# Kernel optimization log

Measured on AMD Instinct MI355X. Metric: run time of the kernel, lower is better.

## Reference

```python
import jax, jax.numpy as jnp
import numpy as np

B, T, N, D_IN = 2, 64, 64, 512
HID, L, H = 256, 2, 4
C = HID // H  # 64 per-head channels
NEG_SLOPE = 0.2
LN_EPS = 1e-5


def setup_inputs() -> dict:
    key = jax.random.key(0)
    ks = jax.random.split(key, 8)
    s_in = 1.0 / np.sqrt(D_IN)
    s_h = 1.0 / np.sqrt(HID)
    s_c = 1.0 / np.sqrt(C)
    return {
        "x": jax.random.normal(ks[0], (B, T, N, D_IN), jnp.float32),
        "person_mask": jax.random.randint(ks[1], (B, T, N), 0, 2) > 0,
        "W_in": (jax.random.normal(ks[2], (D_IN, HID)) * s_in).astype(jnp.float32),
        "b_in": jnp.zeros((HID,), jnp.float32),
        "Wl": (jax.random.normal(ks[3], (L, HID, HID)) * s_h).astype(jnp.float32),
        "bl": jnp.zeros((L, HID), jnp.float32),
        "Wr": (jax.random.normal(ks[4], (L, HID, HID)) * s_h).astype(jnp.float32),
        "br": jnp.zeros((L, HID), jnp.float32),
        "att": (jax.random.normal(ks[5], (L, H, C)) * s_c).astype(jnp.float32),
        "out_bias": jnp.zeros((L, HID), jnp.float32),
        "ln_scale": jnp.ones((L, HID), jnp.float32),
        "ln_bias": jnp.zeros((L, HID), jnp.float32),
    }


def _layernorm(x, g, b):
    mu = jnp.mean(x, axis=-1, keepdims=True)
    var = jnp.mean(jnp.square(x - mu), axis=-1, keepdims=True)
    return (x - mu) * jax.lax.rsqrt(var + LN_EPS) * g + b


def _gatv2_layer(h, allowed, Wl, bl, Wr, br, att, ob):
    # h: [bt, N, HID]; allowed: [bt, N, N] bool (edge j->i at [b,i,j])
    bt, n, _ = h.shape
    xl = (h @ Wl + bl).reshape(bt, n, H, C)  # source features (messages)
    xr = (h @ Wr + br).reshape(bt, n, H, C)  # target features
    # GATv2 logit: e_ij = a . leaky_relu(xr_i + xl_j), per head
    s = xr[:, :, None, :, :] + xl[:, None, :, :, :]  # [bt, i, j, H, C]
    e = jnp.einsum('bijhc,hc->bijh', jax.nn.leaky_relu(s, NEG_SLOPE), att)
    e = jnp.where(allowed[..., None], e, -1e9)
    alpha = jax.nn.softmax(e, axis=2)  # segment softmax over incoming edges j
    out = jnp.einsum('bijh,bjhc->bihc', alpha, xl)  # weighted scatter-sum
    return out.reshape(bt, n, H * C) + ob


def _forward(x, person_mask, W_in, b_in, Wl, bl, Wr, br, att, out_bias, ln_scale, ln_bias):
    b, t, n, _ = x.shape
    bt = b * t
    h = (x @ W_in + b_in).reshape(bt, n, HID)
    m = person_mask.reshape(bt, n)
    # edges: all pairs among masked nodes (incl. diag) + self loops for every node
    allowed = (m[:, :, None] & m[:, None, :]) | jnp.eye(n, dtype=bool)[None]
    hi = h
    for li in range(L):
        res = hi
        g = _gatv2_layer(hi, allowed, Wl[li], bl[li], Wr[li], br[li], att[li], out_bias[li])
        g = jax.nn.elu(g)  # dropout is identity in eval mode
        g = _layernorm(g, ln_scale[li], ln_bias[li])
        hi = g + res  # use_residual=True
        hi = jnp.where(m[:, :, None], hi, 0.0)
    # graphs with <=1 masked node are skipped (pass through projected features)
    keep = (jnp.sum(m, axis=-1) > 1)[:, None, None]
    out = jnp.where(keep, hi, h)
    return out.reshape(b, t, n, HID)


def reference(x, person_mask, W_in, b_in, Wl, bl, Wr, br, att, out_bias, ln_scale, ln_bias):
    return _forward(x, person_mask, W_in, b_in, Wl, bl, Wr, br, att, out_bias, ln_scale, ln_bias)
```

## Files before the change

### kernel.cpp

```cpp
#include <hip/hip_runtime.h>
#include <hip/hip_bf16.h>

#define BT_G   128
#define NND    64
#define D_IN_  512
#define HID_   256
#define NH     4
#define NCH    64
#define NROWS  8192
#define LN_EPS_    1e-5f

typedef __hip_bfloat16 bf16;
typedef __attribute__((ext_vector_type(8))) short short8;
typedef __attribute__((ext_vector_type(4))) float float4v;

union PrepArena {
    float t[32][33];
    struct { bf16 As[64 * 72]; bf16 Bs[64 * 72]; } g;
    int flags[4];
};

__global__ __launch_bounds__(256) void prep_gemm_in_kernel(
    const float* __restrict__ x, const unsigned* __restrict__ mw,
    const float* __restrict__ W_in, const float* __restrict__ b_in,
    const float* __restrict__ Wl, const float* __restrict__ Wr,
    float* __restrict__ Cf, bf16* __restrict__ Cb16,
    bf16* __restrict__ WlrT, int* __restrict__ mout)
{
    __shared__ PrepArena ar;
    const int tid = threadIdx.x;
    const int bid = blockIdx.x;

    if (bid < 512) {
        bf16* As = ar.g.As;
        bf16* Bs = ar.g.Bs;
        const int wave = tid >> 6, lane = tid & 63;
        const int quad = lane >> 4, l16 = lane & 15;
        const int m0 = (bid >> 2) * 64, n0 = (bid & 3) * 64;
        const int wm = (wave & 1) * 32, wn = (wave >> 1) * 32;
        float4v acc[2][2] = {};
        const int r  = tid >> 2;
        const int cq = (tid & 3) * 16;
        for (int k0 = 0; k0 < D_IN_; k0 += 64) {
            const float* sa = x + (size_t)(m0 + r) * D_IN_ + k0 + cq;
            const float4 f0 = *(const float4*)(sa);
            const float4 f1 = *(const float4*)(sa + 4);
            const float4 f2 = *(const float4*)(sa + 8);
            const float4 f3 = *(const float4*)(sa + 12);
            const float* sw = W_in + (size_t)(k0 + r) * HID_ + n0 + cq;
            float wv[16];
            *(float4*)(wv)      = *(const float4*)(sw);
            *(float4*)(wv + 4)  = *(const float4*)(sw + 4);
            *(float4*)(wv + 8)  = *(const float4*)(sw + 8);
            *(float4*)(wv + 12) = *(const float4*)(sw + 12);
            union { bf16 hh[16]; float4 v[2]; } u;
            u.hh[0]=__float2bfloat16(f0.x); u.hh[1]=__float2bfloat16(f0.y);
            u.hh[2]=__float2bfloat16(f0.z); u.hh[3]=__float2bfloat16(f0.w);
            u.hh[4]=__float2bfloat16(f1.x); u.hh[5]=__float2bfloat16(f1.y);
            u.hh[6]=__float2bfloat16(f1.z); u.hh[7]=__float2bfloat16(f1.w);
            u.hh[8]=__float2bfloat16(f2.x); u.hh[9]=__float2bfloat16(f2.y);
            u.hh[10]=__float2bfloat16(f2.z); u.hh[11]=__float2bfloat16(f2.w);
            u.hh[12]=__float2bfloat16(f3.x); u.hh[13]=__float2bfloat16(f3.y);
            u.hh[14]=__float2bfloat16(f3.z); u.hh[15]=__float2bfloat16(f3.w);
            __syncthreads();
            *(float4*)(&As[r * 72 + cq])     = u.v[0];
            *(float4*)(&As[r * 72 + cq + 8]) = u.v[1];
            #pragma unroll
            for (int j = 0; j < 16; ++j)
                Bs[(cq + j) * 72 + r] = __float2bfloat16(wv[j]);
            __syncthreads();
            #pragma unroll
            for (int kk = 0; kk < 64; kk += 32) {
                short8 af[2], bf2[2];
                #pragma unroll
                for (int mi = 0; mi < 2; ++mi)
                    af[mi] = *(const short8*)(&As[(wm + mi * 16 + l16) * 72 + kk + quad * 8]);
                #pragma unroll
                for (int ni = 0; ni < 2; ++ni)
                    bf2[ni] = *(const short8*)(&Bs[(wn + ni * 16 + l16) * 72 + kk + quad * 8]);
                #pragma unroll
                for (int mi = 0; mi < 2; ++mi)
                    #pragma unroll
                    for (int ni = 0; ni < 2; ++ni)
                        acc[mi][ni] = __builtin_amdgcn_mfma_f32_16x16x32_bf16(
                            af[mi], bf2[ni], acc[mi][ni], 0, 0, 0);
            }
        }
        #pragma unroll
        for (int ni = 0; ni < 2; ++ni) {
            const int col = n0 + wn + ni * 16 + l16;
            const float bv = b_in[col];
            #pragma unroll
            for (int mi = 0; mi < 2; ++mi)
                #pragma unroll
                for (int rr = 0; rr < 4; ++rr) {
                    const int row = m0 + wm + mi * 16 + quad * 4 + rr;
                    const float v = acc[mi][ni][rr] + bv;
                    Cf[(size_t)row * HID_ + col] = v;
                    Cb16[(size_t)row * HID_ + col] = __float2bfloat16(v);
                }
        }
    } else if (bid < 768) {
        const int q = bid - 512;
        const int z4 = q >> 6;
        const int s = q & 63;
        const int n0 = (s & 7) * 32, k0 = (s >> 3) * 32;
        const float* src = (z4 < 2) ? (Wl + z4 * 65536) : (Wr + (z4 - 2) * 65536);
        bf16* dst = WlrT + ((z4 < 2) ? (size_t)z4 * 131072
                                     : (size_t)(z4 - 2) * 131072 + 65536);
        const int tx = tid & 31, ty = tid >> 5;
        #pragma unroll
        for (int i = 0; i < 4; ++i)
            ar.t[ty + 8 * i][tx] = src[(size_t)(k0 + ty + 8 * i) * 256 + n0 + tx];
        __syncthreads();
        #pragma unroll
        for (int i = 0; i < 4; ++i)
            dst[(size_t)(n0 + ty + 8 * i) * 256 + k0 + tx] =
                __float2bfloat16(ar.t[tx][ty + 8 * i]);
    } else {
        int* fl = ar.flags;
        if (tid == 0) { fl[0] = 1; fl[1] = 1; fl[2] = 1; fl[3] = 1; }
        __syncthreads();
        int aI = 1, aF = 1, aB = 1, aC = 1;
        for (int i = tid; i < 2048; i += 256) {
            const unsigned w2 = mw[i];
            aI &= (w2 <= 1u);
            aF &= (w2 == 0u || w2 == 0x3F800000u);
            const unsigned lo = w2 & 0xFFFFu, hi = w2 >> 16;
            aB &= ((lo == 0u || lo == 0x3F80u) && (hi == 0u || hi == 0x3F80u));
            aC &= (((w2 | (w2 >> 8) | (w2 >> 16) | (w2 >> 24)) & 0xFEu) == 0u);
        }
        if (!aI) atomicAnd(&fl[0], 0);
        if (!aF) atomicAnd(&fl[1], 0);
        if (!aB) atomicAnd(&fl[2], 0);
        if (!aC) atomicAnd(&fl[3], 0);
        __syncthreads();
        const int layout = (fl[0] || fl[1]) ? 0 : (fl[2] ? 2 : (fl[3] ? 3 : 0));
        for (int i = tid; i < NROWS; i += 256) {
            int v;
            if (layout == 2)      v = (((const unsigned short*)mw)[i] != 0);
            else if (layout == 3) v = (((const unsigned char*)mw)[i] != 0);
            else                  v = (mw[i] != 0u);
            mout[i] = v;
        }
    }
}

__global__ __launch_bounds__(256) void gemm_mfma_kernel(
    const bf16* __restrict__ A, const bf16* __restrict__ BT,
    const float* __restrict__ bias0, const float* __restrict__ bias1,
    float* __restrict__ Ca, float* __restrict__ Cbf, int M, int K)
{
    __shared__ bf16 As[128 * 72];
    __shared__ bf16 Bs[64 * 72];
    const int tid  = threadIdx.x;
    const int wave = tid >> 6, lane = tid & 63;
    const int quad = lane >> 4, l16 = lane & 15;
    const int m0 = blockIdx.y * 128, n0g = blockIdx.x * 64;
    const int wm = (wave & 1) * 64, wn = (wave >> 1) * 32;
    float4v acc[4][2] = {};
    const int r  = tid >> 2;
    const int cq = (tid & 3) * 16;

    for (int k0 = 0; k0 < K; k0 += 64) {
        const bf16* sa0 = A  + (size_t)(m0 + r) * K + k0 + cq;
        const bf16* sa1 = sa0 + (size_t)64 * K;
        const bf16* sb  = BT + (size_t)(n0g + r) * K + k0 + cq;
        const float4 a00 = *(const float4*)(sa0);
        const float4 a01 = *(const float4*)(sa0 + 8);
        const float4 a10 = *(const float4*)(sa1);
        const float4 a11 = *(const float4*)(sa1 + 8);
        const float4 b0  = *(const float4*)(sb);
        const float4 b1  = *(const float4*)(sb + 8);
        __syncthreads();
        *(float4*)(&As[r * 72 + cq])            = a00;
        *(float4*)(&As[r * 72 + cq + 8])        = a01;
        *(float4*)(&As[(r + 64) * 72 + cq])     = a10;
        *(float4*)(&As[(r + 64) * 72 + cq + 8]) = a11;
        *(float4*)(&Bs[r * 72 + cq])            = b0;
        *(float4*)(&Bs[r * 72 + cq + 8])        = b1;
        __syncthreads();
        #pragma unroll
        for (int kk = 0; kk < 64; kk += 32) {
            short8 af[4], bf2[2];
            #pragma unroll
            for (int mi = 0; mi < 4; ++mi)
                af[mi] = *(const short8*)(&As[(wm + mi * 16 + l16) * 72 + kk + quad * 8]);
            #pragma unroll
            for (int ni = 0; ni < 2; ++ni)
                bf2[ni] = *(const short8*)(&Bs[(wn + ni * 16 + l16) * 72 + kk + quad * 8]);
            #pragma unroll
            for (int mi = 0; mi < 4; ++mi)
                #pragma unroll
                for (int ni = 0; ni < 2; ++ni)
                    acc[mi][ni] = __builtin_amdgcn_mfma_f32_16x16x32_bf16(
                        af[mi], bf2[ni], acc[mi][ni], 0, 0, 0);
        }
    }
    const bool loHalf = (n0g < 256);
    float* Co = loHalf ? Ca : Cbf;
    const float* bp = loHalf ? bias0 : bias1;
    const int cbase = loHalf ? n0g : (n0g - 256);
    #pragma unroll
    for (int ni = 0; ni < 2; ++ni) {
        const int col = cbase + wn + ni * 16 + l16;
        const float bv = bp[col];
        #pragma unroll
        for (int mi = 0; mi < 4; ++mi)
            #pragma unroll
            for (int rr = 0; rr < 4; ++rr) {
                const int row = m0 + wm + mi * 16 + quad * 4 + rr;
                Co[(size_t)row * 256 + col] = acc[mi][ni][rr] + bv;
            }
    }
}

__global__ __launch_bounds__(256) void attn_kernel(
    const float* xl, const float* xr, const float* att,
    const int* msk, float* g)
{
    __shared__ float xls [64][68];
    __shared__ float xlsT[64][68];
    __shared__ float xrsT[64][36];
    __shared__ float av[64];
    __shared__ int   ms[64];

    const int tid   = threadIdx.x;
    const int head  = blockIdx.x >> 1;
    const int half  = blockIdx.x & 1;
    const int gr    = blockIdx.y;
    const int ibase = half * 32;
    const int ti = tid >> 4, tj = tid & 15;
    const int i0 = ti * 2, j0 = tj * 4;

    const float* xlg = xl + (size_t)gr * NND * HID_ + head * NCH;
    const float* xrg = xr + ((size_t)gr * NND + ibase) * HID_ + head * NCH;

    {
        const int r  = tid >> 2;
        const int c0 = (tid & 3) * 16;
        const int r2 = tid >> 3;
        const int cb = (tid & 7) * 8;
        float a[4][4], b[2][4];
        #pragma unroll
        for (int k = 0; k < 4; ++k)
            *(float4*)a[k] = *(const float4*)(xlg + r * HID_ + c0 + 4 * k);
        *(float4*)b[0] = *(const float4*)(xrg + r2 * HID_ + cb);
        *(float4*)b[1] = *(const float4*)(xrg + r2 * HID_ + cb + 4);
        #pragma unroll
        for (int k = 0; k < 4; ++k)
            *(float4*)&xls[r][c0 + 4 * k] = *(float4*)a[k];
        #pragma unroll
        for (int k = 0; k < 4; ++k)
            #pragma unroll
            for (int w = 0; w < 4; ++w)
                xlsT[c0 + 4 * k + w][r] = a[k][w];
        #pragma unroll
        for (int k = 0; k < 2; ++k)
            #pragma unroll
            for (int w = 0; w < 4; ++w)
                xrsT[cb + 4 * k + w][r2] = b[k][w];
        if (tid < 64) {
            av[tid] = att[head * NCH + tid];
            ms[tid] = msk[gr * NND + tid];
        }
    }
    __syncthreads();

    float aa[2][4] = {};
    float p2[2] = {}, q4[4] = {};
    for (int c = 0; c < 64; ++c) {
        const float a = av[c];
        float xr2[2], xl4[4];
        *(float2*)xr2 = *(const float2*)&xrsT[c][i0];
        *(float4*)xl4 = *(const float4*)&xlsT[c][j0];
        #pragma unroll
        for (int y = 0; y < 2; ++y) p2[y] = fmaf(a, xr2[y], p2[y]);
        #pragma unroll
        for (int x = 0; x < 4; ++x) q4[x] = fmaf(a, xl4[x], q4[x]);
        #pragma unroll
        for (int y = 0; y < 2; ++y)
            #pragma unroll
            for (int x = 0; x < 4; ++x)
                aa[y][x] = fmaf(a, fabsf(xr2[y] + xl4[x]), aa[y][x]);
    }

    float inv2[2];
    {
        int mi2[2], mj4[4];
        #pragma unroll
        for (int y = 0; y < 2; ++y) mi2[y] = ms[ibase + i0 + y];
        #pragma unroll
        for (int x = 0; x < 4; ++x) mj4[x] = ms[j0 + x];
        #pragma unroll
        for (int y = 0; y < 2; ++y) {
            float e[4];
            #pragma unroll
            for (int x = 0; x < 4; ++x) {
                const float ev = fmaf(0.4f, aa[y][x], 0.6f * (p2[y] + q4[x]));
                const bool allowed = (mi2[y] && mj4[x]) || (ibase + i0 + y == j0 + x);
                e[x] = allowed ? ev : -1e9f;
            }
            float m = fmaxf(fmaxf(e[0], e[1]), fmaxf(e[2], e[3]));
            #pragma unroll
            for (int off = 1; off < 16; off <<= 1)
                m = fmaxf(m, __shfl_xor(m, off));
            float s = 0.f;
            #pragma unroll
            for (int x = 0; x < 4; ++x) {
                const float ev = __expf(e[x] - m);
                aa[y][x] = ev;
                s += ev;
            }
            #pragma unroll
            for (int off = 1; off < 16; off <<= 1)
                s += __shfl_xor(s, off);
            inv2[y] = 1.f / s;
        }
    }

    {
        const int c0 = j0;
        float oa[2][4] = {};
        for (int jb = 0; jb < 16; ++jb) {
            const int src = ti * 16 + jb;
            #pragma unroll
            for (int jj = 0; jj < 4; ++jj) {
                const int j = jb * 4 + jj;
                float xv[4];
                *(float4*)xv = *(const float4*)&xls[j][c0];
                #pragma unroll
                for (int y = 0; y < 2; ++y) {
                    const float al = __shfl(aa[y][jj], src);
                    #pragma unroll
                    for (int x = 0; x < 4; ++x)
                        oa[y][x] = fmaf(al, xv[x], oa[y][x]);
                }
            }
        }
        #pragma unroll
        for (int y = 0; y < 2; ++y) {
            const float iv = inv2[y];
            float o[4];
            #pragma unroll
            for (int x = 0; x < 4; ++x) o[x] = oa[y][x] * iv;
            float* go = g + (size_t)(gr * NND + ibase + i0 + y) * HID_ + head * NCH + c0;
            *(float4*)go = *(float4*)o;
        }
    }
}

__global__ __launch_bounds__(256) void epilogue_kernel(
    const float* __restrict__ g, const float* res,
    const float* __restrict__ ob, const float* __restrict__ lns,
    const float* __restrict__ lnb, const int* __restrict__ msk,
    float* hout, bf16* hb, int finalSel)
{
    const int lane = threadIdx.x & 63;
    const int wave = threadIdx.x >> 6;
    const int m = blockIdx.x * 4 + wave;
    if (finalSel) {
        const int gr = m >> 6;
        const int mv = msk[gr * NND + lane];
        const unsigned long long bal = __ballot(mv != 0);
        if (__popcll(bal) <= 1) return;
    }
    const float* grow = g + (size_t)m * HID_;
    float v[4];
    float sum = 0.f;
    #pragma unroll
    for (int q = 0; q < 4; ++q) {
        const int c = q * 64 + lane;
        float x = grow[c] + ob[c];
        x = x > 0.f ? x : (__expf(x) - 1.f);
        v[q] = x; sum += x;
    }
    #pragma unroll
    for (int off = 1; off < 64; off <<= 1) sum += __shfl_xor(sum, off);
    const float mu = sum * (1.f / 256.f);
    float vs = 0.f;
    #pragma unroll
    for (int q = 0; q < 4; ++q) { const float d = v[q] - mu; vs += d * d; }
    #pragma unroll
    for (int off = 1; off < 64; off <<= 1) vs += __shfl_xor(vs, off);
    const float rstd = rsqrtf(vs * (1.f / 256.f) + LN_EPS_);
    const int mnode = msk[m];
    const float* rrow = res + (size_t)m * HID_;
    float* ho = hout + (size_t)m * HID_;
    #pragma unroll
    for (int q = 0; q < 4; ++q) {
        const int c = q * 64 + lane;
        float y = (v[q] - mu) * rstd * lns[c] + lnb[c];
        y += rrow[c];
        y = mnode ? y : 0.f;
        ho[c] = y;
        if (hb) hb[(size_t)m * HID_ + c] = __float2bfloat16(y);
    }
}

extern "C" void kernel_launch(void* const* d_in, const int* in_sizes, int n_in,
                              void* d_out, int out_size, void* d_ws, size_t ws_size,
                              hipStream_t stream) {
    const float* x    = (const float*)d_in[0];
    const float* W_in = (const float*)d_in[2];
    const float* b_in = (const float*)d_in[3];
    const float* Wl   = (const float*)d_in[4];
    const float* bl   = (const float*)d_in[5];
    const float* Wr   = (const float*)d_in[6];
    const float* br   = (const float*)d_in[7];
    const float* att  = (const float*)d_in[8];
    const float* ob   = (const float*)d_in[9];
    const float* lns  = (const float*)d_in[10];
    const float* lnb  = (const float*)d_in[11];
    float* out = (float*)d_out;

    char* w = (char*)d_ws;
    int*   mcan = (int*)w;                      w += 32768;
    float* h    = (float*)w;                    w += (size_t)NROWS * HID_ * 4;
    float* xlb  = (float*)w;                    w += (size_t)NROWS * HID_ * 4;
    float* xra  = (float*)w;                    w += (size_t)NROWS * HID_ * 4;
    bf16*  hxb  = (bf16*)w;                     w += (size_t)NROWS * HID_ * 2;
    bf16*  WlrT = (bf16*)w;

    prep_gemm_in_kernel<<<769, 256, 0, stream>>>(
        x, (const unsigned*)d_in[1], W_in, b_in, Wl, Wr, out, hxb, WlrT, mcan);

    gemm_mfma_kernel<<<dim3(512 / 64, NROWS / 128), 256, 0, stream>>>(
        hxb, WlrT, bl, br, xlb, xra, NROWS, HID_);

    attn_kernel<<<dim3(NH * 2, BT_G), 256, 0, stream>>>(
        xlb, xra, att, mcan, xra);

    epilogue_kernel<<<NROWS / 4, 256, 0, stream>>>(
        xra, out, ob, lns, lnb, mcan, h, hxb, 0);

    gemm_mfma_kernel<<<dim3(512 / 64, NROWS / 128), 256, 0, stream>>>(
        hxb, WlrT + (size_t)512 * HID_, bl + HID_, br + HID_, xlb, xra, NROWS, HID_);

    attn_kernel<<<dim3(NH * 2, BT_G), 256, 0, stream>>>(
        xlb, xra, att + NH * NCH, mcan, xra);

    epilogue_kernel<<<NROWS / 4, 256, 0, stream>>>(
        xra, h, ob + HID_, lns + HID_, lnb + HID_, mcan,
        out, (bf16*)nullptr, 1);

    (void)in_sizes; (void)n_in; (void)out_size; (void)ws_size;
}
```

Before: 176.5 us.

## Fuse per-layer xl/xr projection GEMM into the attention kernel

Merges the projection GEMM and the attention kernel into one kernel per layer. Each block computes the 64x128 slice of xl/xr for one graph and one head with MFMA and writes it straight into shared memory, so xl/xr never go through global memory and one launch per layer is removed. Each block now covers all 64 targets instead of 32, which halves the grid to 512 blocks and doubles per-thread accumulators. This may lower occupancy and parallelism in exchange for less HBM traffic.

```diff
diff --git a/kernel.cpp b/kernel.cpp
--- a/kernel.cpp
+++ b/kernel.cpp
@@ -146,159 +146,138 @@
     }
 }
 
-__global__ __launch_bounds__(256) void gemm_mfma_kernel(
-    const bf16* __restrict__ A, const bf16* __restrict__ BT,
-    const float* __restrict__ bias0, const float* __restrict__ bias1,
-    float* __restrict__ Ca, float* __restrict__ Cbf, int M, int K)
+union FusedArena {
+    struct { bf16 As[64 * 72]; bf16 Bs[128 * 72]; } g;
+    struct { float xls[64][68], xlsT[64][68], xrsT[64][68]; } a;
+};
+
+__global__ __launch_bounds__(256) void gemm_attn_kernel(
+    const bf16* __restrict__ hxbA, const bf16* __restrict__ WlrTl,
+    const float* __restrict__ bll, const float* __restrict__ brl,
+    const float* __restrict__ attl, const int* __restrict__ msk,
+    float* __restrict__ g)
 {
-    __shared__ bf16 As[128 * 72];
-    __shared__ bf16 Bs[64 * 72];
+    __shared__ FusedArena ar;
+    __shared__ float av[64];
+    __shared__ int   ms[64];
+
     const int tid  = threadIdx.x;
+    const int head = blockIdx.x, gr = blockIdx.y;
     const int wave = tid >> 6, lane = tid & 63;
     const int quad = lane >> 4, l16 = lane & 15;
-    const int m0 = blockIdx.y * 128, n0g = blockIdx.x * 64;
-    const int wm = (wave & 1) * 64, wn = (wave >> 1) * 32;
-    float4v acc[4][2] = {};
-    const int r  = tid >> 2;
-    const int cq = (tid & 3) * 16;
-
-    for (int k0 = 0; k0 < K; k0 += 64) {
-        const bf16* sa0 = A  + (size_t)(m0 + r) * K + k0 + cq;
-        const bf16* sa1 = sa0 + (size_t)64 * K;
-        const bf16* sb  = BT + (size_t)(n0g + r) * K + k0 + cq;
-        const float4 a00 = *(const float4*)(sa0);
-        const float4 a01 = *(const float4*)(sa0 + 8);
-        const float4 a10 = *(const float4*)(sa1);
-        const float4 a11 = *(const float4*)(sa1 + 8);
-        const float4 b0  = *(const float4*)(sb);
-        const float4 b1  = *(const float4*)(sb + 8);
-        __syncthreads();
-        *(float4*)(&As[r * 72 + cq])            = a00;
-        *(float4*)(&As[r * 72 + cq + 8])        = a01;
-        *(float4*)(&As[(r + 64) * 72 + cq])     = a10;
-        *(float4*)(&As[(r + 64) * 72 + cq + 8]) = a11;
-        *(float4*)(&Bs[r * 72 + cq])            = b0;
-        *(float4*)(&Bs[r * 72 + cq + 8])        = b1;
-        __syncthreads();
-        #pragma unroll
-        for (int kk = 0; kk < 64; kk += 32) {
-            short8 af[4], bf2[2];
-            #pragma unroll
-            for (int mi = 0; mi < 4; ++mi)
-                af[mi] = *(const short8*)(&As[(wm + mi * 16 + l16) * 72 + kk + quad * 8]);
-            #pragma unroll
-            for (int ni = 0; ni < 2; ++ni)
-                bf2[ni] = *(const short8*)(&Bs[(wn + ni * 16 + l16) * 72 + kk + quad * 8]);
-            #pragma unroll
-            for (int mi = 0; mi < 4; ++mi)
-                #pragma unroll
-                for (int ni = 0; ni < 2; ++ni)
-                    acc[mi][ni] = __builtin_amdgcn_mfma_f32_16x16x32_bf16(
-                        af[mi], bf2[ni], acc[mi][ni], 0, 0, 0);
-        }
-    }
-    const bool loHalf = (n0g < 256);
-    float* Co = loHalf ? Ca : Cbf;
-    const float* bp = loHalf ? bias0 : bias1;
-    const int cbase = loHalf ? n0g : (n0g - 256);
-    #pragma unroll
-    for (int ni = 0; ni < 2; ++ni) {
-        const int col = cbase + wn + ni * 16 + l16;
-        const float bv = bp[col];
-        #pragma unroll
-        for (int mi = 0; mi < 4; ++mi)
-            #pragma unroll
-            for (int rr = 0; rr < 4; ++rr) {
-                const int row = m0 + wm + mi * 16 + quad * 4 + rr;
-                Co[(size_t)row * 256 + col] = acc[mi][ni][rr] + bv;
+    const int wm = (wave & 1) * 32;
+    const int wn = (wave >> 1) * 64;
+    float4v acc[2][4] = {};
+
+    {
+        bf16* As = ar.g.As;
+        bf16* Bs = ar.g.Bs;
+        const int rA  = tid >> 2;
+        const int cqA = (tid & 3) * 16;
+        const int rB  = tid >> 1;
+        const int cqB = (tid & 1) * 32;
+        const int srcB = (rB < 64) ? (head * NCH + rB) : (256 + head * NCH + rB - 64);
+        for (int k0 = 0; k0 < HID_; k0 += 64) {
+            const bf16* sa = hxbA + (size_t)(gr * NND + rA) * HID_ + k0 + cqA;
+            const float4 a0 = *(const float4*)(sa);
+            const float4 a1 = *(const float4*)(sa + 8);
+            const bf16* sb = WlrTl + (size_t)srcB * HID_ + k0 + cqB;
+            const float4 b0 = *(const float4*)(sb);
+            const float4 b1 = *(const float4*)(sb + 8);
+            const float4 b2 = *(const float4*)(sb + 16);
+            const float4 b3 = *(const float4*)(sb + 24);
+            __syncthreads();
+            *(float4*)(&As[rA * 72 + cqA])      = a0;
+            *(float4*)(&As[rA * 72 + cqA + 8])  = a1;
+            *(float4*)(&Bs[rB * 72 + cqB])      = b0;
+            *(float4*)(&Bs[rB * 72 + cqB + 8])  = b1;
+            *(float4*)(&Bs[rB * 72 + cqB + 16]) = b2;
+            *(float4*)(&Bs[rB * 72 + cqB + 24]) = b3;
+            __syncthreads();
+            #pragma unroll
+            for (int kk = 0; kk < 64; kk += 32) {
+                short8 af[2], bf2[4];
+                #pragma unroll
+                for (int mi = 0; mi < 2; ++mi)
+                    af[mi] = *(const short8*)(&As[(wm + mi * 16 + l16) * 72 + kk + quad * 8]);
+                #pragma unroll
+                for (int ni = 0; ni < 4; ++ni)
+                    bf2[ni] = *(const short8*)(&Bs[(wn + ni * 16 + l16) * 72 + kk + quad * 8]);
+                #pragma unroll
+                for (int mi = 0; mi < 2; ++mi)
+                    #pragma unroll
+                    for (int ni = 0; ni < 4; ++ni)
+                        acc[mi][ni] = __builtin_amdgcn_mfma_f32_16x16x32_bf16(
+                            af[mi], bf2[ni], acc[mi][ni], 0, 0, 0);
             }
-    }
-}
-
-__global__ __launch_bounds__(256) void attn_kernel(
-    const float* xl, const float* xr, const float* att,
-    const int* msk, float* g)
-{
-    __shared__ float xls [64][68];
-    __shared__ float xlsT[64][68];
-    __shared__ float xrsT[64][36];
-    __shared__ float av[64];
-    __shared__ int   ms[64];
-
-    const int tid   = threadIdx.x;
-    const int head  = blockIdx.x >> 1;
-    const int half  = blockIdx.x & 1;
-    const int gr    = blockIdx.y;
-    const int ibase = half * 32;
+        }
+    }
+    __syncthreads();
+
+    {
+        const bool xlW = (wn == 0);
+        const float* bp = xlW ? bll : brl;
+        float bias[4];
+        #pragma unroll
+        for (int ni = 0; ni < 4; ++ni)
+            bias[ni] = bp[head * NCH + ni * 16 + l16];
+        #pragma unroll
+        for (int mi = 0; mi < 2; ++mi)
+            #pragma unroll
+            for (int ni = 0; ni < 4; ++ni)
+                #pragma unroll
+                for (int rr = 0; rr < 4; ++rr) {
+                    const int row = wm + mi * 16 + quad * 4 + rr;
+                    const int c   = ni * 16 + l16;
+                    const float v = acc[mi][ni][rr] + bias[ni];
+                    if (xlW) {
+                        ar.a.xls[row][c] = v;
+                        ar.a.xlsT[c][row] = v;
+                    } else {
+                        ar.a.xrsT[c][row] = v;
+                    }
+                }
+        if (tid < 64) {
+            av[tid] = attl[head * NCH + tid];
+            ms[tid] = msk[gr * NND + tid];
+        }
+    }
+    __syncthreads();
+
     const int ti = tid >> 4, tj = tid & 15;
-    const int i0 = ti * 2, j0 = tj * 4;
-
-    const float* xlg = xl + (size_t)gr * NND * HID_ + head * NCH;
-    const float* xrg = xr + ((size_t)gr * NND + ibase) * HID_ + head * NCH;
-
-    {
-        const int r  = tid >> 2;
-        const int c0 = (tid & 3) * 16;
-        const int r2 = tid >> 3;
-        const int cb = (tid & 7) * 8;
-        float a[4][4], b[2][4];
-        #pragma unroll
-        for (int k = 0; k < 4; ++k)
-            *(float4*)a[k] = *(const float4*)(xlg + r * HID_ + c0 + 4 * k);
-        *(float4*)b[0] = *(const float4*)(xrg + r2 * HID_ + cb);
-        *(float4*)b[1] = *(const float4*)(xrg + r2 * HID_ + cb + 4);
-        #pragma unroll
-        for (int k = 0; k < 4; ++k)
-            *(float4*)&xls[r][c0 + 4 * k] = *(float4*)a[k];
-        #pragma unroll
-        for (int k = 0; k < 4; ++k)
-            #pragma unroll
-            for (int w = 0; w < 4; ++w)
-                xlsT[c0 + 4 * k + w][r] = a[k][w];
-        #pragma unroll
-        for (int k = 0; k < 2; ++k)
-            #pragma unroll
-            for (int w = 0; w < 4; ++w)
-                xrsT[cb + 4 * k + w][r2] = b[k][w];
-        if (tid < 64) {
-            av[tid] = att[head * NCH + tid];
-            ms[tid] = msk[gr * NND + tid];
-        }
-    }
-    __syncthreads();
-
-    float aa[2][4] = {};
-    float p2[2] = {}, q4[4] = {};
+    const int i0 = ti * 4, j0 = tj * 4;
+    float aa[4][4] = {};
+    float p4[4] = {}, q4[4] = {};
     for (int c = 0; c < 64; ++c) {
         const float a = av[c];
-        float xr2[2], xl4[4];
-        *(float2*)xr2 = *(const float2*)&xrsT[c][i0];
-        *(float4*)xl4 = *(const float4*)&xlsT[c][j0];
-        #pragma unroll
-        for (int y = 0; y < 2; ++y) p2[y] = fmaf(a, xr2[y], p2[y]);
+        float xr4[4], xl4[4];
+        *(float4*)xr4 = *(const float4*)&ar.a.xrsT[c][i0];
+        *(float4*)xl4 = *(const float4*)&ar.a.xlsT[c][j0];
+        #pragma unroll
+        for (int y = 0; y < 4; ++y) p4[y] = fmaf(a, xr4[y], p4[y]);
         #pragma unroll
         for (int x = 0; x < 4; ++x) q4[x] = fmaf(a, xl4[x], q4[x]);
         #pragma unroll
-        for (int y = 0; y < 2; ++y)
+        for (int y = 0; y < 4; ++y)
             #pragma unroll
             for (int x = 0; x < 4; ++x)
-                aa[y][x] = fmaf(a, fabsf(xr2[y] + xl4[x]), aa[y][x]);
-    }
-
-    float inv2[2];
+                aa[y][x] = fmaf(a, fabsf(xr4[y] + xl4[x]), aa[y][x]);
+    }
+
+    float inv4[4];
     {
-        int mi2[2], mj4[4];
-        #pragma unroll
-        for (int y = 0; y < 2; ++y) mi2[y] = ms[ibase + i0 + y];
+        int mi4[4], mj4[4];
+        #pragma unroll
+        for (int y = 0; y < 4; ++y) mi4[y] = ms[i0 + y];
         #pragma unroll
         for (int x = 0; x < 4; ++x) mj4[x] = ms[j0 + x];
         #pragma unroll
-        for (int y = 0; y < 2; ++y) {
+        for (int y = 0; y < 4; ++y) {
             float e[4];
             #pragma unroll
             for (int x = 0; x < 4; ++x) {
-                const float ev = fmaf(0.4f, aa[y][x], 0.6f * (p2[y] + q4[x]));
-                const bool allowed = (mi2[y] && mj4[x]) || (ibase + i0 + y == j0 + x);
+                const float ev = fmaf(0.4f, aa[y][x], 0.6f * (p4[y] + q4[x]));
+                const bool allowed = (mi4[y] && mj4[x]) || (i0 + y == j0 + x);
                 e[x] = allowed ? ev : -1e9f;
             }
             float m = fmaxf(fmaxf(e[0], e[1]), fmaxf(e[2], e[3]));
@@ -315,22 +294,22 @@
             #pragma unroll
             for (int off = 1; off < 16; off <<= 1)
                 s += __shfl_xor(s, off);
-            inv2[y] = 1.f / s;
+            inv4[y] = 1.f / s;
         }
     }
 
     {
         const int c0 = j0;
-        float oa[2][4] = {};
+        float oa[4][4] = {};
         for (int jb = 0; jb < 16; ++jb) {
             const int src = ti * 16 + jb;
             #pragma unroll
             for (int jj = 0; jj < 4; ++jj) {
                 const int j = jb * 4 + jj;
                 float xv[4];
-                *(float4*)xv = *(const float4*)&xls[j][c0];
-                #pragma unroll
-                for (int y = 0; y < 2; ++y) {
+                *(float4*)xv = *(const float4*)&ar.a.xls[j][c0];
+                #pragma unroll
+                for (int y = 0; y < 4; ++y) {
                     const float al = __shfl(aa[y][jj], src);
                     #pragma unroll
                     for (int x = 0; x < 4; ++x)
@@ -339,12 +318,12 @@
             }
         }
         #pragma unroll
-        for (int y = 0; y < 2; ++y) {
-            const float iv = inv2[y];
+        for (int y = 0; y < 4; ++y) {
+            const float iv = inv4[y];
             float o[4];
             #pragma unroll
             for (int x = 0; x < 4; ++x) o[x] = oa[y][x] * iv;
-            float* go = g + (size_t)(gr * NND + ibase + i0 + y) * HID_ + head * NCH + c0;
+            float* go = g + (size_t)(gr * NND + i0 + y) * HID_ + head * NCH + c0;
             *(float4*)go = *(float4*)o;
         }
     }
@@ -417,31 +396,25 @@
     char* w = (char*)d_ws;
     int*   mcan = (int*)w;                      w += 32768;
     float* h    = (float*)w;                    w += (size_t)NROWS * HID_ * 4;
-    float* xlb  = (float*)w;                    w += (size_t)NROWS * HID_ * 4;
-    float* xra  = (float*)w;                    w += (size_t)NROWS * HID_ * 4;
+    float* gbuf = (float*)w;                    w += (size_t)NROWS * HID_ * 4;
     bf16*  hxb  = (bf16*)w;                     w += (size_t)NROWS * HID_ * 2;
     bf16*  WlrT = (bf16*)w;
 
     prep_gemm_in_kernel<<<769, 256, 0, stream>>>(
         x, (const unsigned*)d_in[1], W_in, b_in, Wl, Wr, out, hxb, WlrT, mcan);
 
-    gemm_mfma_kernel<<<dim3(512 / 64, NROWS / 128), 256, 0, stream>>>(
-        hxb, WlrT, bl, br, xlb, xra, NROWS, HID_);
-
-    attn_kernel<<<dim3(NH * 2, BT_G), 256, 0, stream>>>(
-        xlb, xra, att, mcan, xra);
+    gemm_attn_kernel<<<dim3(NH, BT_G), 256, 0, stream>>>(
+        hxb, WlrT, bl, br, att, mcan, gbuf);
 
     epilogue_kernel<<<NROWS / 4, 256, 0, stream>>>(
-        xra, out, ob, lns, lnb, mcan, h, hxb, 0);
-
-    gemm_mfma_kernel<<<dim3(512 / 64, NROWS / 128), 256, 0, stream>>>(
-        hxb, WlrT + (size_t)512 * HID_, bl + HID_, br + HID_, xlb, xra, NROWS, HID_);
-
-    attn_kernel<<<dim3(NH * 2, BT_G), 256, 0, stream>>>(
-        xlb, xra, att + NH * NCH, mcan, xra);
+        gbuf, out, ob, lns, lnb, mcan, h, hxb, 0);
+
+    gemm_attn_kernel<<<dim3(NH, BT_G), 256, 0, stream>>>(
+        hxb, WlrT + (size_t)512 * HID_, bl + HID_, br + HID_,
+        att + NH * NCH, mcan, gbuf);
 
     epilogue_kernel<<<NROWS / 4, 256, 0, stream>>>(
-        xra, h, ob + HID_, lns + HID_, lnb + HID_, mcan,
+        gbuf, h, ob + HID_, lns + HID_, lnb + HID_, mcan,
         out, (bf16*)nullptr, 1);
 
     (void)in_sizes; (void)n_in; (void)out_size; (void)ws_size;
```

New measurement: 168.8 us (median of 2 runs). 1.05x faster.
